# Optimization experiments

Hardware: AMD Instinct MI355X
Metric: run time of the kernel (lower is better)

The kernel has to match this reference:

```python
import jax, jax.numpy as jnp
import numpy as np
import itertools

# Buffers from init_kwargs (constants)
N_GRID = (64, 64, 64)
GRID_MIN = 0.0
DX = 1.0 / 64.0
D, H, W = N_GRID[0] + 2, N_GRID[1] + 2, N_GRID[2] + 2  # padded grid 66^3


def setup_inputs() -> dict:
    key = jax.random.key(0)
    k1, k2, k3, k4 = jax.random.split(key, 4)
    B, N, Ci, Co = 2, 200000, 32, 32
    x = jax.random.normal(k1, (B, N, Ci), jnp.float32)
    # positions uniform in [0,1) -> Xp=(pos-grid_min)/dx in [0,64), indices in [0,65]
    pos = jax.random.uniform(k2, (B, N, 3), jnp.float32)
    kernel = jax.random.normal(k3, (3, 3, 3, Ci, Co), jnp.float32) * 0.1
    bias = jax.random.normal(k4, (Co,), jnp.float32) * 0.1
    return {"x": x, "pos": pos, "kernel": kernel, "bias": bias}


def _forward(x, pos, kernel, bias):
    B, N, Ci = x.shape
    Co = kernel.shape[-1]
    Xp = (pos - GRID_MIN) / DX                      # [B,N,3]
    base = Xp.astype(jnp.int32)                     # trunc == floor (Xp >= 0)
    fx = Xp - base.astype(Xp.dtype) - 0.5
    # quadratic B-spline weights: w[..., k, dim], k in {0,1,2}
    w = jnp.stack([0.5 * (0.5 - fx) ** 2,
                   0.75 - fx ** 2,
                   0.5 * (0.5 + fx) ** 2], axis=-2)  # [B,N,3,3]
    base = base + 1
    batch = jnp.arange(B)[:, None]                  # [B,1] for batched scatter
    result = jnp.zeros((B, D * H * W, Co), x.dtype)
    # 27 fixed stencil offsets (structural small loop, not a data-dim loop)
    for oi, oj, ok in itertools.product(range(3), repeat=3):
        weight = w[..., oi, 0] * w[..., oj, 1] * w[..., ok, 2]      # [B,N]
        idx = base + jnp.array([oi, oj, ok], jnp.int32) - 1          # [B,N,3]
        idx1d = idx[..., 0] * (H * W) + idx[..., 1] * W + idx[..., 2]
        vals = weight[..., None] * (x @ kernel[oi, oj, ok] + bias)   # [B,N,Co]
        result = result.at[batch, idx1d].add(vals)
    return result.reshape(B, D, H, W, Co).transpose(0, 4, 1, 2, 3)   # [B,Co,D,H,W]


def reference(x, pos, kernel, bias):
    return _forward(x, pos, kernel, bias)
```

## Files before the change

### kernel.cpp

```cpp
#include <hip/hip_runtime.h>

#define GD   66
#define GHW  (66*66)
#define GDHW (66*66*66)
#define CI   32
#define CO   32

__device__ __forceinline__ void atomAdd(float* p, float v) {
    unsafeAtomicAdd(p, v);
}

template<bool CELLCO>
__global__ __launch_bounds__(256) void p2g_kernel(
    const float* __restrict__ x, const float* __restrict__ pos,
    const float* __restrict__ kern, const float* __restrict__ bias,
    float* __restrict__ dst, int N, int nPairs)
{
    __shared__ float kl[9*32*32];
    const int co   = threadIdx.x & 31;
    const int half = threadIdx.x >> 5;
    const float bco = bias[co];
    const int halvesTotal = gridDim.x * 8;

    for (int oi = 0; oi < 3; ++oi) {
        __syncthreads();
        for (int i = threadIdx.x; i < 9*32*32; i += 256)
            kl[i] = kern[oi*(9*32*32) + i];
        __syncthreads();

        for (int pp = blockIdx.x*8 + half; pp < nPairs; pp += halvesTotal) {
            const int g0 = pp*2;

            float xr[2][32];
            #pragma unroll
            for (int p = 0; p < 2; ++p) {
                const float4* xp = (const float4*)(x + (size_t)(g0+p)*CI);
                #pragma unroll
                for (int i = 0; i < 8; ++i) {
                    float4 v = xp[i];
                    xr[p][4*i+0]=v.x; xr[p][4*i+1]=v.y; xr[p][4*i+2]=v.z; xr[p][4*i+3]=v.w;
                }
            }

            float wxo[2], wy[2][3], wz[2][3];
            int cb[2], bsel[2];
            #pragma unroll
            for (int p = 0; p < 2; ++p) {
                const int gp = g0 + p;
                float px = pos[gp*3+0]*64.f, py = pos[gp*3+1]*64.f, pz = pos[gp*3+2]*64.f;
                int bx = (int)px, by = (int)py, bz = (int)pz;
                float fx = px - bx - 0.5f, fy = py - by - 0.5f, fz = pz - bz - 0.5f;
                float a0 = 0.5f*(0.5f-fx)*(0.5f-fx);
                float a1 = 0.75f - fx*fx;
                float a2 = 0.5f*(0.5f+fx)*(0.5f+fx);
                wxo[p] = (oi==0) ? a0 : ((oi==1) ? a1 : a2);
                wy[p][0]=0.5f*(0.5f-fy)*(0.5f-fy); wy[p][1]=0.75f-fy*fy; wy[p][2]=0.5f*(0.5f+fy)*(0.5f+fy);
                wz[p][0]=0.5f*(0.5f-fz)*(0.5f-fz); wz[p][1]=0.75f-fz*fz; wz[p][2]=0.5f*(0.5f+fz)*(0.5f+fz);
                cb[p]   = (bx+oi)*GHW + by*GD + bz;
                bsel[p] = (gp >= N) ? 1 : 0;
            }

            #pragma unroll
            for (int oj = 0; oj < 3; ++oj) {
                #pragma unroll
                for (int ok = 0; ok < 3; ++ok) {
                    const float* kc = kl + (oj*3+ok)*1024;
                    float y0 = bco, y1 = bco;
                    #pragma unroll
                    for (int ci = 0; ci < 32; ++ci) {
                        float kv = kc[ci*32 + co];
                        y0 += xr[0][ci]*kv;
                        y1 += xr[1][ci]*kv;
                    }
                    {
                        int cell = cb[0] + oj*GD + ok;
                        float w  = wxo[0]*wy[0][oj]*wz[0][ok];
                        size_t a = CELLCO ? (((size_t)bsel[0]*GDHW + cell)*32 + (size_t)co)
                                          : (((size_t)(bsel[0]*32 + co))*GDHW + (size_t)cell);
                        atomAdd(dst + a, w*y0);
                    }
                    {
                        int cell = cb[1] + oj*GD + ok;
                        float w  = wxo[1]*wy[1][oj]*wz[1][ok];
                        size_t a = CELLCO ? (((size_t)bsel[1]*GDHW + cell)*32 + (size_t)co)
                                          : (((size_t)(bsel[1]*32 + co))*GDHW + (size_t)cell);
                        atomAdd(dst + a, w*y1);
                    }
                }
            }
        }
    }
}

__global__ __launch_bounds__(256) void transp_kernel(
    const float* __restrict__ ws, float* __restrict__ out)
{
    __shared__ float tile[32][33];
    const int b     = blockIdx.y;
    const int cell0 = blockIdx.x * 32;
    const int n     = min(32, GDHW - cell0);

    const float* src = ws + ((size_t)b*GDHW + cell0)*32;
    for (int e = threadIdx.x; e < n*32; e += 256)
        tile[e>>5][e&31] = src[e];
    __syncthreads();
    for (int e = threadIdx.x; e < 32*32; e += 256) {
        int c  = e >> 5;
        int cl = e & 31;
        if (cl < n)
            out[((size_t)(b*32 + c))*GDHW + cell0 + cl] = tile[cl][c];
    }
}

extern "C" void kernel_launch(void* const* d_in, const int* in_sizes, int n_in,
                              void* d_out, int out_size, void* d_ws, size_t ws_size,
                              hipStream_t stream) {
    const float* x    = (const float*)d_in[0];
    const float* pos  = (const float*)d_in[1];
    const float* kern = (const float*)d_in[2];
    const float* bias = (const float*)d_in[3];
    float* out = (float*)d_out;

    const int N  = in_sizes[0] / (2*CI);
    const int BN = 2*N;
    const int nPairs = (BN + 1) / 2;

    const size_t wsNeed = (size_t)2 * GDHW * CO * sizeof(float);

    if (ws_size >= wsNeed) {
        float* ws = (float*)d_ws;
        hipMemsetAsync(ws, 0, wsNeed, stream);
        p2g_kernel<true><<<dim3(2048), dim3(256), 0, stream>>>(x, pos, kern, bias, ws, N, nPairs);
        transp_kernel<<<dim3((GDHW + 31)/32, 2), dim3(256), 0, stream>>>(ws, out);
    } else {
        hipMemsetAsync(out, 0, (size_t)out_size * sizeof(float), stream);
        p2g_kernel<false><<<dim3(2048), dim3(256), 0, stream>>>(x, pos, kern, bias, out, N, nPairs);
    }
}
```

Before: 1.232 ms.

## Bin particles into spatial bricks and accumulate the scatter in shared memory

Adds a counting-sort pipeline (histogram, scan, scatter) that groups particles by 4x4x4 brick and batch. A new brick kernel then has each block convolve its particles and accumulate all 27 stencil contributions into a 6x6x6x32 shared-memory halo with LDS atomics. Afterwards each block flushes the non-zero halo values to the global grid with one round of global atomics. The aim is to replace most global atomics with shared-memory ones, at the cost of extra launches, small 64-thread blocks with low occupancy, and per-thread matvecs that read kernel weights from global memory.

New measurement: 2.254 ms. 83.0% more time.

```diff
diff --git a/kernel.cpp b/kernel.cpp
--- a/kernel.cpp
+++ b/kernel.cpp
@@ -6,9 +6,157 @@
 #define CI   32
 #define CO   32
 
+#define NBIN 8192
+#define HAL  6
+#define HCELLS (HAL*HAL*HAL)
+#define SBSZ (HCELLS*33 + 8)
+
 __device__ __forceinline__ void atomAdd(float* p, float v) {
     unsafeAtomicAdd(p, v);
 }
+
+
+__global__ __launch_bounds__(256) void binhist(
+    const float* __restrict__ pos, int* __restrict__ counts, int BN, int N)
+{
+    int g = blockIdx.x * 256 + threadIdx.x;
+    if (g >= BN) return;
+    int bx = (int)(pos[3*g+0] * 64.f);
+    int by = (int)(pos[3*g+1] * 64.f);
+    int bz = (int)(pos[3*g+2] * 64.f);
+    int bin = ((g >= N) << 12) | ((bx >> 2) << 8) | ((by >> 2) << 4) | (bz >> 2);
+    atomicAdd(counts + bin, 1);
+}
+
+__global__ __launch_bounds__(1024) void binscan(
+    const int* __restrict__ counts, int* __restrict__ offs, int* __restrict__ cursor)
+{
+    __shared__ int s[1024];
+    const int t = threadIdx.x;
+    int loc[8]; int sum = 0;
+    #pragma unroll
+    for (int j = 0; j < 8; ++j) { loc[j] = sum; sum += counts[t*8 + j]; }
+    s[t] = sum; __syncthreads();
+    for (int off = 1; off < 1024; off <<= 1) {
+        int v = (t >= off) ? s[t - off] : 0;
+        __syncthreads();
+        s[t] += v;
+        __syncthreads();
+    }
+    int base = (t > 0) ? s[t-1] : 0;
+    #pragma unroll
+    for (int j = 0; j < 8; ++j) { offs[t*8+j] = base + loc[j]; cursor[t*8+j] = base + loc[j]; }
+    if (t == 1023) offs[NBIN] = s[1023];
+}
+
+__global__ __launch_bounds__(256) void binscat(
+    const float* __restrict__ pos, int* __restrict__ cursor,
+    int* __restrict__ sidx, int BN, int N)
+{
+    int g = blockIdx.x * 256 + threadIdx.x;
+    if (g >= BN) return;
+    int bx = (int)(pos[3*g+0] * 64.f);
+    int by = (int)(pos[3*g+1] * 64.f);
+    int bz = (int)(pos[3*g+2] * 64.f);
+    int bin = ((g >= N) << 12) | ((bx >> 2) << 8) | ((by >> 2) << 4) | (bz >> 2);
+    int dst = atomicAdd(cursor + bin, 1);
+    sidx[dst] = g;
+}
+
+
+__global__ __launch_bounds__(64) void p2g_brick(
+    const float* __restrict__ x, const float* __restrict__ pos,
+    const float* __restrict__ kern, const float* __restrict__ bias,
+    const int* __restrict__ sidx, const int* __restrict__ offs,
+    float* __restrict__ ws)
+{
+    __shared__ float sb[SBSZ];
+    const int bid = blockIdx.x;
+    const int p0 = offs[bid], p1 = offs[bid + 1];
+    if (p0 == p1) return;
+    const int batch = bid >> 12;
+    const int br  = bid & 4095;
+    const int gx0 = ((br >> 8) & 15) * 4;
+    const int gy0 = ((br >> 4) & 15) * 4;
+    const int gz0 = (br & 15) * 4;
+
+    for (int e = threadIdx.x; e < SBSZ; e += 64) sb[e] = 0.f;
+    __syncthreads();
+
+    for (int p = p0 + (int)threadIdx.x; p < p1; p += 64) {
+        const int g = sidx[p];
+        const float px = pos[3*g+0]*64.f, py = pos[3*g+1]*64.f, pz = pos[3*g+2]*64.f;
+        const int bx = (int)px, by = (int)py, bz = (int)pz;
+        const float fx = px - bx - 0.5f, fy = py - by - 0.5f, fz = pz - bz - 0.5f;
+        const float wx0 = 0.5f*(0.5f-fx)*(0.5f-fx), wx1 = 0.75f-fx*fx, wx2 = 0.5f*(0.5f+fx)*(0.5f+fx);
+        const float wy0 = 0.5f*(0.5f-fy)*(0.5f-fy), wy1 = 0.75f-fy*fy, wy2 = 0.5f*(0.5f+fy)*(0.5f+fy);
+        const float wz0 = 0.5f*(0.5f-fz)*(0.5f-fz), wz1 = 0.75f-fz*fz, wz2 = 0.5f*(0.5f+fz)*(0.5f+fz);
+        const int lx = bx - gx0, ly = by - gy0, lz = bz - gz0;
+
+        float xr[32];
+        const float4* xp = (const float4*)(x + (size_t)g * CI);
+        #pragma unroll
+        for (int i = 0; i < 8; ++i) {
+            float4 v = xp[i];
+            xr[4*i+0]=v.x; xr[4*i+1]=v.y; xr[4*i+2]=v.z; xr[4*i+3]=v.w;
+        }
+
+        #pragma unroll 1
+        for (int o = 0; o < 27; ++o) {
+            const int oi = o / 9, oj = (o / 3) % 3, ok = o % 3;
+            const float* kb = kern + (size_t)o * 1024;
+            float acc[32];
+            #pragma unroll
+            for (int c = 0; c < 32; ++c) acc[c] = bias[c];
+            #pragma unroll
+            for (int ci = 0; ci < 32; ++ci) {
+                const float xv = xr[ci];
+                #pragma unroll
+                for (int c = 0; c < 32; ++c)
+                    acc[c] = fmaf(kb[ci*32 + c], xv, acc[c]);
+            }
+            const float w = (oi==0 ? wx0 : oi==1 ? wx1 : wx2)
+                          * (oj==0 ? wy0 : oj==1 ? wy1 : wy2)
+                          * (ok==0 ? wz0 : ok==1 ? wz1 : wz2);
+            float* sp = sb + ((lx+oi)*36 + (ly+oj)*6 + (lz+ok)) * 33;
+            #pragma unroll
+            for (int c = 0; c < 32; ++c)
+                atomicAdd(sp + c, w * acc[c]);
+        }
+    }
+    __syncthreads();
+
+    for (int e = threadIdx.x; e < HCELLS * 32; e += 64) {
+        const int cell = e >> 5, c = e & 31;
+        const float v = sb[cell*33 + c];
+        if (v != 0.f) {
+            const int cz = cell % 6, cy = (cell / 6) % 6, cx = cell / 36;
+            atomAdd(ws + ((size_t)batch*GDHW + (size_t)(gx0+cx)*GHW
+                          + (size_t)(gy0+cy)*GD + (gz0+cz)) * 32 + c, v);
+        }
+    }
+}
+
+__global__ __launch_bounds__(256) void transp_kernel(
+    const float* __restrict__ ws, float* __restrict__ out)
+{
+    __shared__ float tile[32][33];
+    const int b     = blockIdx.y;
+    const int cell0 = blockIdx.x * 32;
+    const int n     = min(32, GDHW - cell0);
+
+    const float* src = ws + ((size_t)b*GDHW + cell0)*32;
+    for (int e = threadIdx.x; e < n*32; e += 256)
+        tile[e>>5][e&31] = src[e];
+    __syncthreads();
+    for (int e = threadIdx.x; e < 32*32; e += 256) {
+        int c  = e >> 5;
+        int cl = e & 31;
+        if (cl < n)
+            out[((size_t)(b*32 + c))*GDHW + cell0 + cl] = tile[cl][c];
+    }
+}
+
 
 template<bool CELLCO>
 __global__ __launch_bounds__(256) void p2g_kernel(
@@ -30,7 +178,6 @@
 
         for (int pp = blockIdx.x*8 + half; pp < nPairs; pp += halvesTotal) {
             const int g0 = pp*2;
-
             float xr[2][32];
             #pragma unroll
             for (int p = 0; p < 2; ++p) {
@@ -41,7 +188,6 @@
                     xr[p][4*i+0]=v.x; xr[p][4*i+1]=v.y; xr[p][4*i+2]=v.z; xr[p][4*i+3]=v.w;
                 }
             }
-
             float wxo[2], wy[2][3], wz[2][3];
             int cb[2], bsel[2];
             #pragma unroll
@@ -59,7 +205,6 @@
                 cb[p]   = (bx+oi)*GHW + by*GD + bz;
                 bsel[p] = (gp >= N) ? 1 : 0;
             }
-
             #pragma unroll
             for (int oj = 0; oj < 3; ++oj) {
                 #pragma unroll
@@ -92,26 +237,6 @@
     }
 }
 
-__global__ __launch_bounds__(256) void transp_kernel(
-    const float* __restrict__ ws, float* __restrict__ out)
-{
-    __shared__ float tile[32][33];
-    const int b     = blockIdx.y;
-    const int cell0 = blockIdx.x * 32;
-    const int n     = min(32, GDHW - cell0);
-
-    const float* src = ws + ((size_t)b*GDHW + cell0)*32;
-    for (int e = threadIdx.x; e < n*32; e += 256)
-        tile[e>>5][e&31] = src[e];
-    __syncthreads();
-    for (int e = threadIdx.x; e < 32*32; e += 256) {
-        int c  = e >> 5;
-        int cl = e & 31;
-        if (cl < n)
-            out[((size_t)(b*32 + c))*GDHW + cell0 + cl] = tile[cl][c];
-    }
-}
-
 extern "C" void kernel_launch(void* const* d_in, const int* in_sizes, int n_in,
                               void* d_out, int out_size, void* d_ws, size_t ws_size,
                               hipStream_t stream) {
@@ -123,17 +248,36 @@
 
     const int N  = in_sizes[0] / (2*CI);
     const int BN = 2*N;
-    const int nPairs = (BN + 1) / 2;
-
-    const size_t wsNeed = (size_t)2 * GDHW * CO * sizeof(float);
-
-    if (ws_size >= wsNeed) {
-        float* ws = (float*)d_ws;
-        hipMemsetAsync(ws, 0, wsNeed, stream);
-        p2g_kernel<true><<<dim3(2048), dim3(256), 0, stream>>>(x, pos, kern, bias, ws, N, nPairs);
-        transp_kernel<<<dim3((GDHW + 31)/32, 2), dim3(256), 0, stream>>>(ws, out);
+
+    const size_t GRIDB   = (size_t)2 * GDHW * CO * sizeof(float);
+    const size_t oCounts = GRIDB;
+    const size_t oOffs   = oCounts + 32768;
+    const size_t oCur    = oOffs   + 33024;
+    const size_t oIdx    = oCur    + 32768;
+    const size_t need    = oIdx + (size_t)BN * 4;
+
+    if (ws_size >= need) {
+        char*  w8     = (char*)d_ws;
+        float* wsg    = (float*)w8;
+        int*   counts = (int*)(w8 + oCounts);
+        int*   offs   = (int*)(w8 + oOffs);
+        int*   cursor = (int*)(w8 + oCur);
+        int*   sidxb  = (int*)(w8 + oIdx);
+
+        hipMemsetAsync(counts, 0, 32768, stream);
+        hipMemsetAsync(wsg, 0, GRIDB, stream);
+        binhist<<<dim3((BN + 255)/256), dim3(256), 0, stream>>>(pos, counts, BN, N);
+        binscan<<<dim3(1), dim3(1024), 0, stream>>>(counts, offs, cursor);
+        binscat<<<dim3((BN + 255)/256), dim3(256), 0, stream>>>(pos, cursor, sidxb, BN, N);
+        p2g_brick<<<dim3(NBIN), dim3(64), 0, stream>>>(x, pos, kern, bias, sidxb, offs, wsg);
+        transp_kernel<<<dim3((GDHW + 31)/32, 2), dim3(256), 0, stream>>>(wsg, out);
+    } else if (ws_size >= GRIDB) {
+        float* wsg = (float*)d_ws;
+        hipMemsetAsync(wsg, 0, GRIDB, stream);
+        p2g_kernel<true><<<dim3(2048), dim3(256), 0, stream>>>(x, pos, kern, bias, wsg, N, (BN+1)/2);
+        transp_kernel<<<dim3((GDHW + 31)/32, 2), dim3(256), 0, stream>>>(wsg, out);
     } else {
         hipMemsetAsync(out, 0, (size_t)out_size * sizeof(float), stream);
-        p2g_kernel<false><<<dim3(2048), dim3(256), 0, stream>>>(x, pos, kern, bias, out, N, nPairs);
-    }
-}
+        p2g_kernel<false><<<dim3(2048), dim3(256), 0, stream>>>(x, pos, kern, bias, out, N, (BN+1)/2);
+    }
+}
```
